# Kernel tuning notes

Hardware: AMD Instinct MI355X
Metric: run time of the kernel (lower is better)

Reference implementation:

```python
import jax, jax.numpy as jnp
import numpy as np

B, N, E, DIN, DOUT = 4, 10000, 320000, 128, 128
EPS = 1e-5


def setup_inputs() -> dict:
    key = jax.random.key(0)
    ks = jax.random.split(key, 10)
    x = jax.random.normal(ks[0], (B, N, DIN), dtype=jnp.float32)
    edge_index = jax.random.randint(ks[1], (2, E), 0, N, dtype=jnp.int64)
    norm = jax.random.uniform(ks[2], (E, 1), dtype=jnp.float32)
    W_w = jax.random.normal(ks[3], (DOUT, DIN), dtype=jnp.float32) / np.sqrt(DIN)
    W_b = jax.random.normal(ks[4], (DOUT,), dtype=jnp.float32) * 0.01
    bn_gamma = jnp.ones((N,), dtype=jnp.float32)
    bn_beta = jnp.zeros((N,), dtype=jnp.float32)
    bn_mean = jax.random.normal(ks[5], (N,), dtype=jnp.float32) * 0.01
    bn_var = jax.random.uniform(ks[6], (N,), dtype=jnp.float32, minval=0.5, maxval=1.5)
    return {"x": x, "edge_index": edge_index, "norm": norm, "W_w": W_w,
            "W_b": W_b, "bn_gamma": bn_gamma, "bn_beta": bn_beta,
            "bn_mean": bn_mean, "bn_var": bn_var}


def reference(x, edge_index, norm, W_w, W_b, bn_gamma, bn_beta, bn_mean, bn_var):
    # Dropout is identity in eval mode.
    h = jnp.einsum('bnf,of->bno', x, W_w) + W_b            # [B, N, DOUT]
    # BatchNorm1d over channel dim = node dim (eval mode, running stats)
    inv = jax.lax.rsqrt(bn_var + EPS)
    h = (h - bn_mean[None, :, None]) * (inv * bn_gamma)[None, :, None] + bn_beta[None, :, None]
    h = jax.nn.gelu(h, approximate=False)                  # torch GELU default = exact erf
    # gather -> scale -> scatter-add message passing
    msgs = h[:, edge_index[1], :] * norm                   # [B, E, DOUT]
    out = jnp.zeros_like(h).at[:, edge_index[0], :].add(msgs)
    return out
```

## Files before the change

### kernel.cpp

```cpp
#include <hip/hip_runtime.h>
#include <math.h>

#define DIN 128
#define DOUT 128
#define EPS 1e-5f
#define CHUNK_SHIFT 11
#define CAPC 32

typedef unsigned short ushort_t;
typedef __bf16 bf16x8 __attribute__((ext_vector_type(8)));
typedef float f32x16 __attribute__((ext_vector_type(16)));

__device__ __forceinline__ unsigned int f2bf_u(float f) {
    union { float f; unsigned int i; } v; v.f = f;
    unsigned int x = v.i;
    unsigned int r = x + 0x7fffu + ((x >> 16) & 1u);
    return r >> 16;
}
__device__ __forceinline__ ushort_t f2bf(float f) { return (ushort_t)f2bf_u(f); }

__device__ __forceinline__ float gelu_exact(float v) {
    float ax = fabsf(v) * 0.70710678118654752f;
    float t  = __builtin_amdgcn_rcpf(fmaf(0.3275911f, ax, 1.0f));
    float p  = fmaf(fmaf(fmaf(fmaf(1.061405429f, t, -1.453152027f),
                              t, 1.421413741f),
                         t, -0.284496736f),
                    t, 0.254829592f) * t;
    float e  = __builtin_amdgcn_exp2f(ax * ax * -1.4426950408889634f);
    float erf_ax = fmaf(-p, e, 1.0f);
    float erfv = (v < 0.0f) ? -erf_ax : erf_ax;
    return 0.5f * v * (1.0f + erfv);
}

__global__ __launch_bounds__(256) void prep_kernel(
    const float* __restrict__ W, uint4* __restrict__ wb,
    int* __restrict__ counts, int total_counts)
{
    int t = blockIdx.x * blockDim.x + threadIdx.x;
    if (t < 2048) {
        int ct = t >> 9, kc = (t >> 6) & 7, l = t & 63;
        int o = ct * 32 + (l & 31);
        int f = kc * 16 + ((l >> 5) << 3);
        const float4* src = (const float4*)(W + o * 128 + f);
        float4 v0 = src[0], v1 = src[1];
        uint4 pk;
        pk.x = f2bf_u(v0.x) | (f2bf_u(v0.y) << 16);
        pk.y = f2bf_u(v0.z) | (f2bf_u(v0.w) << 16);
        pk.z = f2bf_u(v1.x) | (f2bf_u(v1.y) << 16);
        pk.w = f2bf_u(v1.z) | (f2bf_u(v1.w) << 16);
        wb[t] = pk;
    }
    for (int i = t; i < total_counts; i += gridDim.x * blockDim.x) counts[i] = 0;
}

__global__ __launch_bounds__(256, 4) void gemm_bn_gelu_fill(
    const float* __restrict__ x, const uint4* __restrict__ wb,
    const float* __restrict__ bias, const float* __restrict__ gamma,
    const float* __restrict__ beta, const float* __restrict__ mean,
    const float* __restrict__ var, ushort_t* __restrict__ hb,
    const int* __restrict__ ei, const float* __restrict__ norm,
    int* __restrict__ counts, unsigned int* __restrict__ csr,
    int N, int E, int nc)
{
    __shared__ ushort_t XH[8192];
    __shared__ float sm_mu[16], sm_sc[16], sm_bt[16];

    const int tid = threadIdx.x;
    const int n0 = blockIdx.x * 16;
    const int w = tid >> 6;
    const int lane = tid & 63;

    bf16x8 bfr[8];
#pragma unroll
    for (int kc = 0; kc < 8; ++kc)
        bfr[kc] = *(const bf16x8*)(wb + (w * 512 + kc * 64 + lane));

    {
        const int gid = blockIdx.x * blockDim.x + tid;
        const int stride = gridDim.x * blockDim.x;
        for (int e = gid; e < E; e += 2 * stride) {
            int ep = e + stride;
            int has2 = ep < E;
            int dst0 = ei[e];
            int src0 = ei[E + e];
            float nm0 = norm[e];
            int dst1 = 0, src1 = 0;
            float nm1 = 0.f;
            if (has2) { dst1 = ei[ep]; src1 = ei[E + ep]; nm1 = norm[ep]; }
            int b0 = dst0 * nc + (src0 >> CHUNK_SHIFT);
            int slot0 = atomicAdd(&counts[b0], 1);
            if (slot0 < CAPC)
                csr[((size_t)b0 << 5) + slot0] =
                    ((unsigned int)src0 << 16) | f2bf_u(nm0);
            if (has2) {
                int b1 = dst1 * nc + (src1 >> CHUNK_SHIFT);
                int slot1 = atomicAdd(&counts[b1], 1);
                if (slot1 < CAPC)
                    csr[((size_t)b1 << 5) + slot1] =
                        ((unsigned int)src1 << 16) | f2bf_u(nm1);
            }
        }
    }

    if (tid < 16) {
        int n = n0 + tid;
        sm_mu[tid] = mean[n];
        sm_sc[tid] = rsqrtf(var[n] + EPS) * gamma[n];
        sm_bt[tid] = beta[n];
    }

#pragma unroll
    for (int it = 0; it < 4; ++it) {
        int tup = tid + it * 256;
        int rt = tup >> 9, kc = (tup >> 6) & 7, l = tup & 63;
        int r = rt * 32 + (l & 31);
        int b = r >> 4, i = r & 15;
        size_t grow = (size_t)b * N + n0 + i;
        int f = kc * 16 + ((l >> 5) << 3);
        const float4* src = (const float4*)(x + grow * 128 + f);
        float4 v0 = src[0], v1 = src[1];
        uint4 pk;
        pk.x = f2bf_u(v0.x) | (f2bf_u(v0.y) << 16);
        pk.y = f2bf_u(v0.z) | (f2bf_u(v0.w) << 16);
        pk.z = f2bf_u(v1.x) | (f2bf_u(v1.y) << 16);
        pk.w = f2bf_u(v1.z) | (f2bf_u(v1.w) << 16);
        *(uint4*)&XH[tup * 8] = pk;
    }
    __syncthreads();

    f32x16 acc0 = {};
    f32x16 acc1 = {};
#pragma unroll
    for (int kc = 0; kc < 8; ++kc) {
        bf16x8 a0 = *(const bf16x8*)&XH[(kc * 64 + lane) * 8];
        bf16x8 a1 = *(const bf16x8*)&XH[(512 * 8) + (kc * 64 + lane) * 8];
        acc0 = __builtin_amdgcn_mfma_f32_32x32x16_bf16(a0, bfr[kc], acc0, 0, 0, 0);
        acc1 = __builtin_amdgcn_mfma_f32_32x32x16_bf16(a1, bfr[kc], acc1, 0, 0, 0);
    }
    __syncthreads();

    const int col = w * 32 + (lane & 31);
    const float bias_c = bias[col];
    const int hi4 = (lane >> 5) * 4;
#pragma unroll
    for (int reg = 0; reg < 8; ++reg) {
        int i0 = (reg & 3) + 8 * (reg >> 2) + hi4;
        float mu = sm_mu[i0], sc = sm_sc[i0], bt = sm_bt[i0];
        float vals[4] = { acc0[reg], acc0[reg + 8], acc1[reg], acc1[reg + 8] };
        ushort4 pk;
        { float v = (vals[0] + bias_c - mu) * sc + bt; pk.x = f2bf(gelu_exact(v)); }
        { float v = (vals[1] + bias_c - mu) * sc + bt; pk.y = f2bf(gelu_exact(v)); }
        { float v = (vals[2] + bias_c - mu) * sc + bt; pk.z = f2bf(gelu_exact(v)); }
        { float v = (vals[3] + bias_c - mu) * sc + bt; pk.w = f2bf(gelu_exact(v)); }
        *(ushort4*)&XH[((i0 << 7) + col) << 2] = pk;
    }
    __syncthreads();

    {
        const float4* s = (const float4*)XH;
        float4* d = (float4*)(hb + (size_t)n0 * 512);
#pragma unroll
        for (int i = tid; i < 1024; i += 256) d[i] = s[i];
    }
}

__device__ __forceinline__ void fma8(float* acc, int4 h, float wgt) {
    union { unsigned int i; float f; } t;
    unsigned int u;
    u = (unsigned int)h.x;
    t.i = u << 16;          acc[0] = fmaf(t.f, wgt, acc[0]);
    t.i = u & 0xffff0000u;  acc[1] = fmaf(t.f, wgt, acc[1]);
    u = (unsigned int)h.y;
    t.i = u << 16;          acc[2] = fmaf(t.f, wgt, acc[2]);
    t.i = u & 0xffff0000u;  acc[3] = fmaf(t.f, wgt, acc[3]);
    u = (unsigned int)h.z;
    t.i = u << 16;          acc[4] = fmaf(t.f, wgt, acc[4]);
    t.i = u & 0xffff0000u;  acc[5] = fmaf(t.f, wgt, acc[5]);
    u = (unsigned int)h.w;
    t.i = u << 16;          acc[6] = fmaf(t.f, wgt, acc[6]);
    t.i = u & 0xffff0000u;  acc[7] = fmaf(t.f, wgt, acc[7]);
}

__device__ __forceinline__ void burst8(const ushort_t* __restrict__ hb,
                                       unsigned int meta, int j, int cnt,
                                       int lane, float* acc)
{
    unsigned int m[8];
#pragma unroll
    for (int k = 0; k < 8; ++k) {
        unsigned int mk =
            (unsigned int)__builtin_amdgcn_readlane((int)meta, j + k);
        m[k] = (j + k < cnt) ? mk : 0u;
    }
    int4 h0 = *(const int4*)(hb + (size_t)(m[0] >> 16) * 512 + lane * 8);
    int4 h1 = *(const int4*)(hb + (size_t)(m[1] >> 16) * 512 + lane * 8);
    int4 h2 = *(const int4*)(hb + (size_t)(m[2] >> 16) * 512 + lane * 8);
    int4 h3 = *(const int4*)(hb + (size_t)(m[3] >> 16) * 512 + lane * 8);
    int4 h4 = *(const int4*)(hb + (size_t)(m[4] >> 16) * 512 + lane * 8);
    int4 h5 = *(const int4*)(hb + (size_t)(m[5] >> 16) * 512 + lane * 8);
    int4 h6 = *(const int4*)(hb + (size_t)(m[6] >> 16) * 512 + lane * 8);
    int4 h7 = *(const int4*)(hb + (size_t)(m[7] >> 16) * 512 + lane * 8);
    union { unsigned int i; float f; } wv;
    wv.i = m[0] << 16; fma8(acc, h0, wv.f);
    wv.i = m[1] << 16; fma8(acc, h1, wv.f);
    wv.i = m[2] << 16; fma8(acc, h2, wv.f);
    wv.i = m[3] << 16; fma8(acc, h3, wv.f);
    wv.i = m[4] << 16; fma8(acc, h4, wv.f);
    wv.i = m[5] << 16; fma8(acc, h5, wv.f);
    wv.i = m[6] << 16; fma8(acc, h6, wv.f);
    wv.i = m[7] << 16; fma8(acc, h7, wv.f);
}

__global__ __launch_bounds__(256, 5) void gather_kernel(
    const ushort_t* __restrict__ hb, const int* __restrict__ counts,
    const unsigned int* __restrict__ csr, float* __restrict__ out,
    int N, int nc)
{
    const int w = threadIdx.x >> 6;
    const int lane = threadIdx.x & 63;
    const int na = blockIdx.x * 8 + w * 2;
    if (na >= N) return;
    const int nb = na + 1;
    const bool hasB = (nb < N);

    float accA[8] = {}, accB[8] = {};
    const int l2 = lane & (CAPC - 1);

    for (int c = 0; c < nc; ++c) {
        const int ia = na * nc + c;
        const int ib = ia + nc;
        int cntA = counts[ia];
        int cntB = hasB ? counts[ib] : 0;
        unsigned int metaA = csr[((size_t)ia << 5) + l2];
        unsigned int metaB = hasB ? csr[((size_t)ib << 5) + l2] : 0u;
        if (cntA > CAPC) cntA = CAPC;
        if (cntB > CAPC) cntB = CAPC;
        for (int j = 0; j < cntA; j += 8) burst8(hb, metaA, j, cntA, lane, accA);
        for (int j = 0; j < cntB; j += 8) burst8(hb, metaB, j, cntB, lane, accB);
    }

    const size_t bstride = (size_t)N * DOUT;
    float* opA = out + (size_t)na * DOUT + lane * 2;
#pragma unroll
    for (int b = 0; b < 4; ++b) {
        float2 v; v.x = accA[b]; v.y = accA[4 + b];
        *(float2*)(opA + b * bstride) = v;
    }
    if (hasB) {
        float* opB = out + (size_t)nb * DOUT + lane * 2;
#pragma unroll
        for (int b = 0; b < 4; ++b) {
            float2 v; v.x = accB[b]; v.y = accB[4 + b];
            *(float2*)(opB + b * bstride) = v;
        }
    }
}

extern "C" void kernel_launch(void* const* d_in, const int* in_sizes, int n_in,
                              void* d_out, int out_size, void* d_ws, size_t ws_size,
                              hipStream_t stream)
{
    const float* x     = (const float*)d_in[0];
    const int*   ei    = (const int*)d_in[1];
    const float* norm  = (const float*)d_in[2];
    const float* W_w   = (const float*)d_in[3];
    const float* W_b   = (const float*)d_in[4];
    const float* gamma = (const float*)d_in[5];
    const float* beta  = (const float*)d_in[6];
    const float* mean  = (const float*)d_in[7];
    const float* var   = (const float*)d_in[8];
    float* out = (float*)d_out;

    const int N = in_sizes[5];
    const int E = in_sizes[2];
    const int nc = (N + (1 << CHUNK_SHIFT) - 1) >> CHUNK_SHIFT;

    ushort_t* hb      = (ushort_t*)d_ws;
    uint4* wb         = (uint4*)(hb + (size_t)N * 512);
    int* counts       = (int*)(wb + 2048);
    unsigned int* csr = (unsigned int*)(counts + (size_t)N * nc);

    int prep_blocks = (N * nc + 255) / 256;
    prep_kernel<<<prep_blocks, 256, 0, stream>>>(W_w, wb, counts, N * nc);

    int gemm_blocks = N / 16;
    gemm_bn_gelu_fill<<<gemm_blocks, 256, 0, stream>>>(
        x, wb, W_b, gamma, beta, mean, var, hb, ei, norm, counts, csr, N, E, nc);

    gather_kernel<<<(N + 7) / 8, 256, 0, stream>>>(hb, counts, csr, out, N, nc);
}
```

Measured before the change: 140.0 us.

## Issue x loads early in GEMM and interleave two nodes' gathers per wave

The GEMM kernel now loads its x tile into registers before the edge-binning loop, so that global load latency overlaps with the atomic CSR fill. The gather kernel now gives each wave four nodes instead of two and processes pairs of nodes together in a dual burst that issues 16 independent row loads at once, raising memory-level parallelism. Occupancy hints drop to 3 blocks per SM for both kernels to make room for the extra registers. The cost is higher register pressure and half as many gather blocks, which may leave fewer waves to hide latency.

```diff
diff --git a/kernel.cpp b/kernel.cpp
--- a/kernel.cpp
+++ b/kernel.cpp
@@ -53,7 +53,7 @@
     for (int i = t; i < total_counts; i += gridDim.x * blockDim.x) counts[i] = 0;
 }
 
-__global__ __launch_bounds__(256, 4) void gemm_bn_gelu_fill(
+__global__ __launch_bounds__(256, 3) void gemm_bn_gelu_fill(
     const float* __restrict__ x, const uint4* __restrict__ wb,
     const float* __restrict__ bias, const float* __restrict__ gamma,
     const float* __restrict__ beta, const float* __restrict__ mean,
@@ -70,10 +70,31 @@
     const int w = tid >> 6;
     const int lane = tid & 63;
 
+    float4 xv[8];
+#pragma unroll
+    for (int it = 0; it < 4; ++it) {
+        int tup = tid + it * 256;
+        int rt = tup >> 9, kc = (tup >> 6) & 7, l = tup & 63;
+        int r = rt * 32 + (l & 31);
+        int b = r >> 4, i = r & 15;
+        size_t grow = (size_t)b * N + n0 + i;
+        int f = kc * 16 + ((l >> 5) << 3);
+        const float4* src = (const float4*)(x + grow * 128 + f);
+        xv[2 * it]     = src[0];
+        xv[2 * it + 1] = src[1];
+    }
+
     bf16x8 bfr[8];
 #pragma unroll
     for (int kc = 0; kc < 8; ++kc)
         bfr[kc] = *(const bf16x8*)(wb + (w * 512 + kc * 64 + lane));
+
+    if (tid < 16) {
+        int n = n0 + tid;
+        sm_mu[tid] = mean[n];
+        sm_sc[tid] = rsqrtf(var[n] + EPS) * gamma[n];
+        sm_bt[tid] = beta[n];
+    }
 
     {
         const int gid = blockIdx.x * blockDim.x + tid;
@@ -102,23 +123,10 @@
         }
     }
 
-    if (tid < 16) {
-        int n = n0 + tid;
-        sm_mu[tid] = mean[n];
-        sm_sc[tid] = rsqrtf(var[n] + EPS) * gamma[n];
-        sm_bt[tid] = beta[n];
-    }
-
 #pragma unroll
     for (int it = 0; it < 4; ++it) {
         int tup = tid + it * 256;
-        int rt = tup >> 9, kc = (tup >> 6) & 7, l = tup & 63;
-        int r = rt * 32 + (l & 31);
-        int b = r >> 4, i = r & 15;
-        size_t grow = (size_t)b * N + n0 + i;
-        int f = kc * 16 + ((l >> 5) << 3);
-        const float4* src = (const float4*)(x + grow * 128 + f);
-        float4 v0 = src[0], v1 = src[1];
+        float4 v0 = xv[2 * it], v1 = xv[2 * it + 1];
         uint4 pk;
         pk.x = f2bf_u(v0.x) | (f2bf_u(v0.y) << 16);
         pk.y = f2bf_u(v0.z) | (f2bf_u(v0.w) << 16);
@@ -181,7 +189,7 @@
     t.i = u & 0xffff0000u;  acc[7] = fmaf(t.f, wgt, acc[7]);
 }
 
-__device__ __forceinline__ void burst8(const ushort_t* __restrict__ hb,
+__device__ __forceinline__ void burst8(const ushort_t* __restrict__ hbp,
                                        unsigned int meta, int j, int cnt,
                                        int lane, float* acc)
 {
@@ -192,14 +200,14 @@
             (unsigned int)__builtin_amdgcn_readlane((int)meta, j + k);
         m[k] = (j + k < cnt) ? mk : 0u;
     }
-    int4 h0 = *(const int4*)(hb + (size_t)(m[0] >> 16) * 512 + lane * 8);
-    int4 h1 = *(const int4*)(hb + (size_t)(m[1] >> 16) * 512 + lane * 8);
-    int4 h2 = *(const int4*)(hb + (size_t)(m[2] >> 16) * 512 + lane * 8);
-    int4 h3 = *(const int4*)(hb + (size_t)(m[3] >> 16) * 512 + lane * 8);
-    int4 h4 = *(const int4*)(hb + (size_t)(m[4] >> 16) * 512 + lane * 8);
-    int4 h5 = *(const int4*)(hb + (size_t)(m[5] >> 16) * 512 + lane * 8);
-    int4 h6 = *(const int4*)(hb + (size_t)(m[6] >> 16) * 512 + lane * 8);
-    int4 h7 = *(const int4*)(hb + (size_t)(m[7] >> 16) * 512 + lane * 8);
+    int4 h0 = *(const int4*)(hbp + (size_t)(m[0] >> 16) * 512 + lane * 8);
+    int4 h1 = *(const int4*)(hbp + (size_t)(m[1] >> 16) * 512 + lane * 8);
+    int4 h2 = *(const int4*)(hbp + (size_t)(m[2] >> 16) * 512 + lane * 8);
+    int4 h3 = *(const int4*)(hbp + (size_t)(m[3] >> 16) * 512 + lane * 8);
+    int4 h4 = *(const int4*)(hbp + (size_t)(m[4] >> 16) * 512 + lane * 8);
+    int4 h5 = *(const int4*)(hbp + (size_t)(m[5] >> 16) * 512 + lane * 8);
+    int4 h6 = *(const int4*)(hbp + (size_t)(m[6] >> 16) * 512 + lane * 8);
+    int4 h7 = *(const int4*)(hbp + (size_t)(m[7] >> 16) * 512 + lane * 8);
     union { unsigned int i; float f; } wv;
     wv.i = m[0] << 16; fma8(acc, h0, wv.f);
     wv.i = m[1] << 16; fma8(acc, h1, wv.f);
@@ -211,47 +219,117 @@
     wv.i = m[7] << 16; fma8(acc, h7, wv.f);
 }
 
-__global__ __launch_bounds__(256, 5) void gather_kernel(
+__device__ __forceinline__ void dual8(const ushort_t* __restrict__ hbp,
+                                      unsigned int mA, int jA, int cA, float* aA,
+                                      unsigned int mB, int jB, int cB, float* aB,
+                                      int lane)
+{
+    unsigned int a[8], b[8];
+#pragma unroll
+    for (int k = 0; k < 8; ++k) {
+        unsigned int v =
+            (unsigned int)__builtin_amdgcn_readlane((int)mA, jA + k);
+        a[k] = (jA + k < cA) ? v : 0u;
+    }
+#pragma unroll
+    for (int k = 0; k < 8; ++k) {
+        unsigned int v =
+            (unsigned int)__builtin_amdgcn_readlane((int)mB, jB + k);
+        b[k] = (jB + k < cB) ? v : 0u;
+    }
+    int4 hA0 = *(const int4*)(hbp + (size_t)(a[0] >> 16) * 512 + lane * 8);
+    int4 hA1 = *(const int4*)(hbp + (size_t)(a[1] >> 16) * 512 + lane * 8);
+    int4 hA2 = *(const int4*)(hbp + (size_t)(a[2] >> 16) * 512 + lane * 8);
+    int4 hA3 = *(const int4*)(hbp + (size_t)(a[3] >> 16) * 512 + lane * 8);
+    int4 hA4 = *(const int4*)(hbp + (size_t)(a[4] >> 16) * 512 + lane * 8);
+    int4 hA5 = *(const int4*)(hbp + (size_t)(a[5] >> 16) * 512 + lane * 8);
+    int4 hA6 = *(const int4*)(hbp + (size_t)(a[6] >> 16) * 512 + lane * 8);
+    int4 hA7 = *(const int4*)(hbp + (size_t)(a[7] >> 16) * 512 + lane * 8);
+    int4 hB0 = *(const int4*)(hbp + (size_t)(b[0] >> 16) * 512 + lane * 8);
+    int4 hB1 = *(const int4*)(hbp + (size_t)(b[1] >> 16) * 512 + lane * 8);
+    int4 hB2 = *(const int4*)(hbp + (size_t)(b[2] >> 16) * 512 + lane * 8);
+    int4 hB3 = *(const int4*)(hbp + (size_t)(b[3] >> 16) * 512 + lane * 8);
+    int4 hB4 = *(const int4*)(hbp + (size_t)(b[4] >> 16) * 512 + lane * 8);
+    int4 hB5 = *(const int4*)(hbp + (size_t)(b[5] >> 16) * 512 + lane * 8);
+    int4 hB6 = *(const int4*)(hbp + (size_t)(b[6] >> 16) * 512 + lane * 8);
+    int4 hB7 = *(const int4*)(hbp + (size_t)(b[7] >> 16) * 512 + lane * 8);
+    union { unsigned int i; float f; } wv;
+    wv.i = a[0] << 16; fma8(aA, hA0, wv.f);
+    wv.i = a[1] << 16; fma8(aA, hA1, wv.f);
+    wv.i = a[2] << 16; fma8(aA, hA2, wv.f);
+    wv.i = a[3] << 16; fma8(aA, hA3, wv.f);
+    wv.i = a[4] << 16; fma8(aA, hA4, wv.f);
+    wv.i = a[5] << 16; fma8(aA, hA5, wv.f);
+    wv.i = a[6] << 16; fma8(aA, hA6, wv.f);
+    wv.i = a[7] << 16; fma8(aA, hA7, wv.f);
+    wv.i = b[0] << 16; fma8(aB, hB0, wv.f);
+    wv.i = b[1] << 16; fma8(aB, hB1, wv.f);
+    wv.i = b[2] << 16; fma8(aB, hB2, wv.f);
+    wv.i = b[3] << 16; fma8(aB, hB3, wv.f);
+    wv.i = b[4] << 16; fma8(aB, hB4, wv.f);
+    wv.i = b[5] << 16; fma8(aB, hB5, wv.f);
+    wv.i = b[6] << 16; fma8(aB, hB6, wv.f);
+    wv.i = b[7] << 16; fma8(aB, hB7, wv.f);
+}
+
+__global__ __launch_bounds__(256, 3) void gather_kernel(
     const ushort_t* __restrict__ hb, const int* __restrict__ counts,
     const unsigned int* __restrict__ csr, float* __restrict__ out,
     int N, int nc)
 {
     const int w = threadIdx.x >> 6;
     const int lane = threadIdx.x & 63;
-    const int na = blockIdx.x * 8 + w * 2;
-    if (na >= N) return;
-    const int nb = na + 1;
-    const bool hasB = (nb < N);
-
-    float accA[8] = {}, accB[8] = {};
-    const int l2 = lane & (CAPC - 1);
+    const int n0 = (blockIdx.x * 4 + w) * 4;
+    if (n0 >= N) return;
+    const int l2 = lane & 31;
+
+    float acc[4][8] = {};
 
     for (int c = 0; c < nc; ++c) {
-        const int ia = na * nc + c;
-        const int ib = ia + nc;
-        int cntA = counts[ia];
-        int cntB = hasB ? counts[ib] : 0;
-        unsigned int metaA = csr[((size_t)ia << 5) + l2];
-        unsigned int metaB = hasB ? csr[((size_t)ib << 5) + l2] : 0u;
-        if (cntA > CAPC) cntA = CAPC;
-        if (cntB > CAPC) cntB = CAPC;
-        for (int j = 0; j < cntA; j += 8) burst8(hb, metaA, j, cntA, lane, accA);
-        for (int j = 0; j < cntB; j += 8) burst8(hb, metaB, j, cntB, lane, accB);
+        int cq[4];
+        unsigned int mq[4];
+#pragma unroll
+        for (int q = 0; q < 4; ++q) {
+            int n = n0 + q;
+            bool ok = (n < N);
+            int idx = (ok ? n : n0) * nc + c;
+            int cv = counts[idx];
+            cq[q] = ok ? (cv > CAPC ? CAPC : cv) : 0;
+            mq[q] = csr[((size_t)idx << 5) + l2];
+        }
+        {
+            int jA = 0, jB = 0;
+            while (jA < cq[0] && jB < cq[1]) {
+                dual8(hb, mq[0], jA, cq[0], acc[0],
+                          mq[1], jB, cq[1], acc[1], lane);
+                jA += 8; jB += 8;
+            }
+            while (jA < cq[0]) { burst8(hb, mq[0], jA, cq[0], lane, acc[0]); jA += 8; }
+            while (jB < cq[1]) { burst8(hb, mq[1], jB, cq[1], lane, acc[1]); jB += 8; }
+        }
+        {
+            int jA = 0, jB = 0;
+            while (jA < cq[2] && jB < cq[3]) {
+                dual8(hb, mq[2], jA, cq[2], acc[2],
+                          mq[3], jB, cq[3], acc[3], lane);
+                jA += 8; jB += 8;
+            }
+            while (jA < cq[2]) { burst8(hb, mq[2], jA, cq[2], lane, acc[2]); jA += 8; }
+            while (jB < cq[3]) { burst8(hb, mq[3], jB, cq[3], lane, acc[3]); jB += 8; }
+        }
     }
 
     const size_t bstride = (size_t)N * DOUT;
-    float* opA = out + (size_t)na * DOUT + lane * 2;
-#pragma unroll
-    for (int b = 0; b < 4; ++b) {
-        float2 v; v.x = accA[b]; v.y = accA[4 + b];
-        *(float2*)(opA + b * bstride) = v;
-    }
-    if (hasB) {
-        float* opB = out + (size_t)nb * DOUT + lane * 2;
-#pragma unroll
-        for (int b = 0; b < 4; ++b) {
-            float2 v; v.x = accB[b]; v.y = accB[4 + b];
-            *(float2*)(opB + b * bstride) = v;
+#pragma unroll
+    for (int q = 0; q < 4; ++q) {
+        int n = n0 + q;
+        if (n < N) {
+            float* op = out + (size_t)n * DOUT + lane * 2;
+#pragma unroll
+            for (int b = 0; b < 4; ++b) {
+                float2 v; v.x = acc[q][b]; v.y = acc[q][4 + b];
+                *(float2*)(op + b * bstride) = v;
+            }
         }
     }
 }
@@ -287,5 +365,6 @@
     gemm_bn_gelu_fill<<<gemm_blocks, 256, 0, stream>>>(
         x, wb, W_b, gamma, beta, mean, var, hb, ei, norm, counts, csr, N, E, nc);
 
-    gather_kernel<<<(N + 7) / 8, 256, 0, stream>>>(hb, counts, csr, out, N, nc);
-}
+    int gather_blocks = (N + 15) / 16;
+    gather_kernel<<<gather_blocks, 256, 0, stream>>>(hb, counts, csr, out, N, nc);
+}
```

Result: no change. 138.9 us (-0.8%).
